# Kernel optimization log

Hardware: AMD Instinct MI355X
Metric: run time of the kernel (lower is better)

The kernel has to match this reference:

```python
import jax, jax.numpy as jnp
import numpy as np

ANCHORS = np.array([[10,13],[16,30],[33,23],[30,61],[62,45],[59,119],[116,90],[156,198],[373,326]], np.float32)
ANCHOR_MASK = [[6, 7, 8], [3, 4, 5], [0, 1, 2]]
INPUT_SHAPE = np.array([416, 416], np.float32)  # (h, w)
NUM_CLASSES = 80
EPS = 1e-7


def _bce(pred, target):
    # clip_by_tensor + binary cross entropy, as in the torch module
    p = jnp.clip(pred, EPS, 1.0 - EPS)
    return -target * jnp.log(p) - (1.0 - target) * jnp.log(1.0 - p)


def _box_iou(b1, b2):
    # b1: (..., 1, 4), b2: (..., n, 4), center-format xywh (normalized)
    b1_xy, b1_wh = b1[..., :2], b1[..., 2:4]
    b2_xy, b2_wh = b2[..., :2], b2[..., 2:4]
    b1_min, b1_max = b1_xy - b1_wh / 2.0, b1_xy + b1_wh / 2.0
    b2_min, b2_max = b2_xy - b2_wh / 2.0, b2_xy + b2_wh / 2.0
    inter_wh = jnp.maximum(jnp.minimum(b1_max, b2_max) - jnp.maximum(b1_min, b2_min), 0.0)
    inter = inter_wh[..., 0] * inter_wh[..., 1]
    a1 = b1_wh[..., 0] * b1_wh[..., 1]
    a2 = b2_wh[..., 0] * b2_wh[..., 1]
    return inter / (a1 + a2 - inter)


def _decode(y_pred, anchors):
    # y_pred: (b, 3*(5+C), h, w) -> raw: (b, 3, h, w, 5+C)
    b, _, h, w = y_pred.shape
    raw = y_pred.reshape(b, 3, 5 + NUM_CLASSES, h, w).transpose(0, 1, 3, 4, 2)
    gy, gx = jnp.meshgrid(jnp.arange(h, dtype=y_pred.dtype), jnp.arange(w, dtype=y_pred.dtype), indexing='ij')
    grid_xy = jnp.stack([gx, gy], axis=-1)  # (h, w, 2)
    pred_xy = jax.nn.sigmoid(raw[..., 0:2])
    pred_wh = raw[..., 2:4]                 # raw tw, th (MSE'd against log target)
    pred_conf = jax.nn.sigmoid(raw[..., 4:5])
    pred_class = jax.nn.sigmoid(raw[..., 5:])
    # decoded, normalized boxes for IoU-based negative mining
    box_xy = (pred_xy + grid_xy) / jnp.array([w, h], y_pred.dtype)
    box_wh = jnp.exp(pred_wh) * anchors.reshape(3, 1, 1, 2) / jnp.asarray(INPUT_SHAPE[::-1].copy())
    pred_box = jnp.concatenate([box_xy, box_wh], axis=-1)  # (b,3,h,w,4)
    return grid_xy, pred_box, pred_xy, pred_wh, pred_conf, pred_class


def _layer_loss(y_pred, y_true, target, anchors):
    b, _, h, w = y_pred.shape
    grid_xy, pred_box, pred_xy, pred_wh, pred_conf, pred_class = _decode(y_pred, anchors)
    object_mask = y_true[..., 4:5]
    true_xy = y_true[..., 0:2] * jnp.array([h, w], y_pred.dtype) - grid_xy
    true_wh = jnp.log(y_true[..., 2:4] * jnp.asarray(INPUT_SHAPE[::-1].copy()) / anchors.reshape(3, 1, 1, 2))
    true_wh = jnp.where(object_mask > 0, true_wh, jnp.zeros_like(true_wh))
    loss_scale = 2.0 - y_true[..., 2:3] * y_true[..., 3:4]
    # negative mask: every grid/anchor prediction vs all true boxes of its image (vectorized over batch)
    iou = _box_iou(pred_box[:, :, :, :, None, :], target[:, None, None, None, :, :4])  # (b,3,h,w,n)
    best_iou = jnp.max(iou, axis=-1)
    neg = (best_iou < 0.5).astype(y_pred.dtype)[..., None]
    neg_mask = (1.0 - object_mask) * neg
    loss_xy = jnp.sum(object_mask * loss_scale * _bce(pred_xy, true_xy))
    loss_wh = jnp.sum(object_mask * loss_scale * 0.5 * (pred_wh - true_wh) ** 2)
    conf_bce = _bce(pred_conf, object_mask)
    loss_conf = jnp.sum(object_mask * conf_bce) + jnp.sum(neg_mask * conf_bce)
    loss_cls = jnp.sum(object_mask * _bce(pred_class, y_true[..., 5:]))
    return loss_xy + loss_wh + loss_conf + loss_cls


def setup_inputs() -> dict:
    key = jax.random.key(0)
    ks = jax.random.split(key, 7)
    grids = [13, 26, 52]
    b, n = 32, 20
    inp = {}
    for i, g in enumerate(grids):
        inp[f'y_pred{i}'] = jax.random.normal(ks[i], (b, 3 * (5 + NUM_CLASSES), g, g), jnp.float32)
        # y_true values in (0.05, 0.95): keeps log(true_wh) and 1/y_true grads bounded
        inp[f'y_true{i}'] = 0.05 + 0.9 * jax.random.uniform(ks[3 + i], (b, 3, g, g, 5 + NUM_CLASSES), jnp.float32)
    inp['target'] = 0.05 + 0.9 * jax.random.uniform(ks[6], (b, n, 5), jnp.float32)
    return inp


def reference(y_pred0, y_pred1, y_pred2, y_true0, y_true1, y_true2, target):
    total = jnp.zeros((), jnp.float32)
    for yp, yt, mask in ((y_pred0, y_true0, ANCHOR_MASK[0]),
                         (y_pred1, y_true1, ANCHOR_MASK[1]),
                         (y_pred2, y_true2, ANCHOR_MASK[2])):
        total = total + _layer_loss(yp, yt, target, jnp.asarray(ANCHORS[mask]))
    return total
```

## Files before the change

### kernel.cpp

```cpp
#include <hip/hip_runtime.h>
#include <math.h>

#define BLOCK 256
#define NB0 64
#define NB1 254
#define NB2 1014
#define NBLOCKS (NB0 + NB1 + NB2)

typedef float f4a __attribute__((ext_vector_type(4), aligned(4)));

__constant__ float c_anch[9][2] = {
    {116.f, 90.f}, {156.f, 198.f}, {373.f, 326.f},
    { 30.f, 61.f}, { 62.f,  45.f}, { 59.f, 119.f},
    { 10.f, 13.f}, { 16.f,  30.f}, { 33.f,  23.f}
};

__device__ __forceinline__ float softplusf(float x) {
    float ax = fabsf(x);
    return fmaxf(x, 0.f) + __logf(1.f + __expf(-ax));
}

__device__ __forceinline__ float sigmoidf(float x) {
    return __fdividef(1.f, 1.f + __expf(-x));
}

__global__ __launch_bounds__(BLOCK, 8) void yolo_loss_main(
    const float* __restrict__ p0, const float* __restrict__ p1, const float* __restrict__ p2,
    const float* __restrict__ t0, const float* __restrict__ t1, const float* __restrict__ t2,
    const float* __restrict__ tgt, float* __restrict__ partials)
{
    __shared__ float sh[BLOCK][17];

    int blk = blockIdx.x;
    const float* pred;
    const float* tru;
    int layer, g, cells, bbase;
    if (blk < NB0)            { layer = 0; pred = p0; tru = t0; g = 13; cells = 16224;  bbase = 0; }
    else if (blk < NB0 + NB1) { layer = 1; pred = p1; tru = t1; g = 26; cells = 64896;  bbase = NB0; }
    else                      { layer = 2; pred = p2; tru = t2; g = 52; cells = 259584; bbase = NB0 + NB1; }

    int tid = threadIdx.x;
    int cell0 = (blk - bbase) * BLOCK;
    int idx = cell0 + tid;
    bool active = idx < cells;
    int nvalid = min(BLOCK, cells - cell0);
    const float* trow = tru + (size_t)cell0 * 85;

#pragma unroll
    for (int k = 0; k < 5; k++) {
        int f = k * BLOCK + tid;
        int cell = f / 5;
        int ch = f - cell * 5;
        int cc = min(cell, nvalid - 1);
        sh[cell][ch] = trow[(size_t)cc * 85 + ch];
    }
    __syncthreads();

    int cidx = active ? idx : (cells - 1);
    int hw = g * g;
    int ij = cidx % hw;
    int a  = (cidx / hw) % 3;
    int b  = cidx / (3 * hw);
    int i  = ij / g;
    int j  = ij - i * g;
    const float* pb = pred + (size_t)((b * 3 + a) * 85) * hw + ij;

    float acc = 0.f;
    float mask = 0.f;

    if (active) {
        float y0 = sh[tid][0], y1 = sh[tid][1], y2 = sh[tid][2], y3 = sh[tid][3];
        mask = sh[tid][4];

        float r0 = pb[0];
        float r1 = pb[hw];
        float r2 = pb[2 * hw];
        float r3 = pb[3 * hw];
        float r4 = pb[4 * hw];

        float gf = (float)g, gx = (float)j, gy = (float)i;
        float aw = c_anch[layer * 3 + a][0];
        float ah = c_anch[layer * 3 + a][1];

        float true_x = y0 * gf - gx;
        float true_y = y1 * gf - gy;
        float ls = 2.f - y2 * y3;
        float lxy = (softplusf(r0) - true_x * r0) + (softplusf(r1) - true_y * r1);
        acc += mask * ls * lxy;

        float tw = __logf(y2 * (416.f / aw));
        float th = __logf(y3 * (416.f / ah));
        float dw = r2 - tw, dh = r3 - th;
        acc += mask * ls * 0.5f * (dw * dw + dh * dh);

        float cbce = softplusf(r4) - mask * r4;

        float sx = sigmoidf(r0);
        float sy = sigmoidf(r1);
        float bx = __fdividef(sx + gx, gf);
        float by = __fdividef(sy + gy, gf);
        float bw = __expf(r2) * aw * (1.f / 416.f);
        float bh = __expf(r3) * ah * (1.f / 416.f);
        float a1 = bw * bh;
        float b1minx = bx - 0.5f * bw, b1maxx = bx + 0.5f * bw;
        float b1miny = by - 0.5f * bh, b1maxy = by + 0.5f * bh;

        const float* tg = tgt + b * 20 * 5;
        float best = 0.f;
#pragma unroll 5
        for (int k = 0; k < 20; k++) {
            f4a t = *reinterpret_cast<const f4a*>(tg + k * 5);
            float hw2 = 0.5f * t.z, hh2 = 0.5f * t.w;
            float iw = fminf(b1maxx, t.x + hw2) - fmaxf(b1minx, t.x - hw2);
            float ih = fminf(b1maxy, t.y + hh2) - fmaxf(b1miny, t.y - hh2);
            iw = fmaxf(iw, 0.f);
            ih = fmaxf(ih, 0.f);
            float inter = iw * ih;
            float iou = __fdividef(inter, a1 + t.z * t.w - inter);
            best = fmaxf(best, iou);
        }
        float neg = (best < 0.5f) ? 1.f : 0.f;
        acc += mask * cbce + (1.f - mask) * neg * cbce;
    }

    float cls = 0.f;
    for (int q = 0; q < 5; q++) {
        __syncthreads();
#pragma unroll
        for (int k = 0; k < 16; k++) {
            int f = k * BLOCK + tid;
            int cell = f >> 4;
            int ch = f & 15;
            int cc = min(cell, nvalid - 1);
            sh[cell][ch] = trow[(size_t)cc * 85 + 5 + q * 16 + ch];
        }
        __syncthreads();
        if (active) {
#pragma unroll
            for (int c = 0; c < 16; c++) {
                float x = pb[(size_t)(5 + q * 16 + c) * hw];
                float t = sh[tid][c];
                cls += softplusf(x) - t * x;
            }
        }
    }
    if (active) acc += mask * cls;

    for (int off = 32; off > 0; off >>= 1)
        acc += __shfl_down(acc, off, 64);
    __shared__ float shr[BLOCK / 64];
    if ((threadIdx.x & 63) == 0)
        shr[threadIdx.x >> 6] = acc;
    __syncthreads();
    if (threadIdx.x == 0) {
        float s = 0.f;
        for (int wv = 0; wv < BLOCK / 64; wv++) s += shr[wv];
        partials[blockIdx.x] = s;
    }
}

__global__ __launch_bounds__(BLOCK) void yolo_loss_reduce(
    const float* __restrict__ partials, float* __restrict__ out)
{
    float s = 0.f;
    for (int i = threadIdx.x; i < NBLOCKS; i += BLOCK)
        s += partials[i];
    for (int off = 32; off > 0; off >>= 1)
        s += __shfl_down(s, off, 64);
    __shared__ float sh[BLOCK / 64];
    if ((threadIdx.x & 63) == 0)
        sh[threadIdx.x >> 6] = s;
    __syncthreads();
    if (threadIdx.x == 0) {
        float tot = 0.f;
        for (int wv = 0; wv < BLOCK / 64; wv++) tot += sh[wv];
        out[0] = tot;
    }
}

extern "C" void kernel_launch(void* const* d_in, const int* in_sizes, int n_in,
                              void* d_out, int out_size, void* d_ws, size_t ws_size,
                              hipStream_t stream) {
    const float* p0  = (const float*)d_in[0];
    const float* t0  = (const float*)d_in[1];
    const float* p1  = (const float*)d_in[2];
    const float* t1  = (const float*)d_in[3];
    const float* p2  = (const float*)d_in[4];
    const float* t2  = (const float*)d_in[5];
    const float* tgt = (const float*)d_in[6];
    float* partials  = (float*)d_ws;

    yolo_loss_main<<<NBLOCKS, BLOCK, 0, stream>>>(p0, p1, p2, t0, t1, t2, tgt, partials);
    yolo_loss_reduce<<<1, BLOCK, 0, stream>>>(partials, (float*)d_out);
}
```

Before: 288.1 us.

## Software-pipeline y_true staging with register prefetch and double-buffered LDS

Restructures the y_true loading into six 16-channel stages, issuing global loads for the next stage into registers while the current stage is consumed from a second shared-memory buffer. This hides global load latency behind the class-loss compute and cuts the number of barriers per stage. In exchange it uses more registers and twice the LDS, and the launch bound drops from 8 to 4 blocks per CU, which lowers occupancy.

```diff
diff --git a/kernel.cpp b/kernel.cpp
--- a/kernel.cpp
+++ b/kernel.cpp
@@ -24,12 +24,56 @@
     return __fdividef(1.f, 1.f + __expf(-x));
 }
 
-__global__ __launch_bounds__(BLOCK, 8) void yolo_loss_main(
+
+template<int Q>
+__device__ __forceinline__ void stage_issue(const float* __restrict__ trow,
+                                            int tid, int nvalid, float* reg) {
+    constexpr int nch = (Q == 5) ? 5 : 16;
+#pragma unroll
+    for (int k = 0; k < nch; k++) {
+        int f = k * BLOCK + tid;
+        int cell = (Q == 5) ? (f / 5) : (f >> 4);
+        int ch = f - cell * nch;
+        int cc = min(cell, nvalid - 1);
+        reg[k] = trow[(size_t)cc * 85 + Q * 16 + ch];
+    }
+}
+
+template<int Q>
+__device__ __forceinline__ void stage_write(float (&sh)[BLOCK][17], int tid,
+                                            const float* reg) {
+    constexpr int nch = (Q == 5) ? 5 : 16;
+#pragma unroll
+    for (int k = 0; k < nch; k++) {
+        int f = k * BLOCK + tid;
+        int cell = (Q == 5) ? (f / 5) : (f >> 4);
+        int ch = f - cell * nch;
+        sh[cell][ch] = reg[k];
+    }
+}
+
+template<int Q>
+__device__ __forceinline__ float consume_cls(const float (&sh)[BLOCK][17],
+                                             const float* __restrict__ pb,
+                                             int tid, int hw) {
+    constexpr int nch = (Q == 5) ? 5 : 16;
+    float cls = 0.f;
+#pragma unroll
+    for (int c = 0; c < nch; c++) {
+        float x = pb[(size_t)(Q * 16 + c) * hw];
+        float t = sh[tid][c];
+        cls += softplusf(x) - t * x;
+    }
+    return cls;
+}
+
+__global__ __launch_bounds__(BLOCK, 4) void yolo_loss_main(
     const float* __restrict__ p0, const float* __restrict__ p1, const float* __restrict__ p2,
     const float* __restrict__ t0, const float* __restrict__ t1, const float* __restrict__ t2,
     const float* __restrict__ tgt, float* __restrict__ partials)
 {
-    __shared__ float sh[BLOCK][17];
+    __shared__ float shA[BLOCK][17];
+    __shared__ float shB[BLOCK][17];
 
     int blk = blockIdx.x;
     const float* pred;
@@ -45,16 +89,6 @@
     bool active = idx < cells;
     int nvalid = min(BLOCK, cells - cell0);
     const float* trow = tru + (size_t)cell0 * 85;
-
-#pragma unroll
-    for (int k = 0; k < 5; k++) {
-        int f = k * BLOCK + tid;
-        int cell = f / 5;
-        int ch = f - cell * 5;
-        int cc = min(cell, nvalid - 1);
-        sh[cell][ch] = trow[(size_t)cc * 85 + ch];
-    }
-    __syncthreads();
 
     int cidx = active ? idx : (cells - 1);
     int hw = g * g;
@@ -65,12 +99,19 @@
     int j  = ij - i * g;
     const float* pb = pred + (size_t)((b * 3 + a) * 85) * hw + ij;
 
-    float acc = 0.f;
-    float mask = 0.f;
-
+    float rA[16], rB[16];
+
+    stage_issue<0>(trow, tid, nvalid, rA);
+    stage_issue<1>(trow, tid, nvalid, rB);
+    stage_write<0>(shA, tid, rA);
+    __syncthreads();
+
+    float acc = 0.f, cls = 0.f, mask = 0.f;
+
+    stage_issue<2>(trow, tid, nvalid, rA);
     if (active) {
-        float y0 = sh[tid][0], y1 = sh[tid][1], y2 = sh[tid][2], y3 = sh[tid][3];
-        mask = sh[tid][4];
+        float y0 = shA[tid][0], y1 = shA[tid][1], y2 = shA[tid][2], y3 = shA[tid][3];
+        mask = shA[tid][4];
 
         float r0 = pb[0];
         float r1 = pb[hw];
@@ -121,30 +162,40 @@
         }
         float neg = (best < 0.5f) ? 1.f : 0.f;
         acc += mask * cbce + (1.f - mask) * neg * cbce;
-    }
-
-    float cls = 0.f;
-    for (int q = 0; q < 5; q++) {
-        __syncthreads();
-#pragma unroll
-        for (int k = 0; k < 16; k++) {
-            int f = k * BLOCK + tid;
-            int cell = f >> 4;
-            int ch = f & 15;
-            int cc = min(cell, nvalid - 1);
-            sh[cell][ch] = trow[(size_t)cc * 85 + 5 + q * 16 + ch];
+
+#pragma unroll
+        for (int c = 5; c < 16; c++) {
+            float x = pb[(size_t)c * hw];
+            float t = shA[tid][c];
+            cls += softplusf(x) - t * x;
         }
-        __syncthreads();
-        if (active) {
-#pragma unroll
-            for (int c = 0; c < 16; c++) {
-                float x = pb[(size_t)(5 + q * 16 + c) * hw];
-                float t = sh[tid][c];
-                cls += softplusf(x) - t * x;
-            }
-        }
-    }
-    if (active) acc += mask * cls;
+    }
+    stage_write<1>(shB, tid, rB);
+    __syncthreads();
+
+    stage_issue<3>(trow, tid, nvalid, rB);
+    if (active) cls += consume_cls<1>(shB, pb, tid, hw);
+    stage_write<2>(shA, tid, rA);
+    __syncthreads();
+
+    stage_issue<4>(trow, tid, nvalid, rA);
+    if (active) cls += consume_cls<2>(shA, pb, tid, hw);
+    stage_write<3>(shB, tid, rB);
+    __syncthreads();
+
+    stage_issue<5>(trow, tid, nvalid, rB);
+    if (active) cls += consume_cls<3>(shB, pb, tid, hw);
+    stage_write<4>(shA, tid, rA);
+    __syncthreads();
+
+    if (active) cls += consume_cls<4>(shA, pb, tid, hw);
+    stage_write<5>(shB, tid, rB);
+    __syncthreads();
+
+    if (active) {
+        cls += consume_cls<5>(shB, pb, tid, hw);
+        acc += mask * cls;
+    }
 
     for (int off = 32; off > 0; off >>= 1)
         acc += __shfl_down(acc, off, 64);
```

After: 275.5 us. -4.4%, faster.

## Stage class targets per wavefront with register prefetch instead of block barriers

Applied to the files above, without the earlier changes.

Each 64-lane wavefront now stages its own slice of y_true in a private shared-memory tile, so the per-chunk block-wide __syncthreads are gone. The next 16-channel class chunk is loaded into registers while the current chunk is consumed, overlapping global loads with the softplus work. Full wavefronts get an unclamped fast path for the strided reads. The register prefetch raises register pressure, so the launch-bounds occupancy hint drops from 8 to 6 blocks, and correctness now depends on in-wavefront ordering of LDS accesses without explicit barriers.

```diff
diff --git a/kernel.cpp b/kernel.cpp
--- a/kernel.cpp
+++ b/kernel.cpp
@@ -24,12 +24,50 @@
     return __fdividef(1.f, 1.f + __expf(-x));
 }
 
-__global__ __launch_bounds__(BLOCK, 8) void yolo_loss_main(
+
+template<int Q>
+__device__ __forceinline__ void stage_cls(const float* __restrict__ tw, int lane,
+                                          int nvc, bool full, float* r) {
+    if (full) {
+        int lo = (lane >> 4) * 85 + (lane & 15);
+#pragma unroll
+        for (int k = 0; k < 16; k++)
+            r[k] = tw[lo + k * 340 + 5 + Q * 16];
+    } else {
+#pragma unroll
+        for (int k = 0; k < 16; k++) {
+            int cc = min(k * 4 + (lane >> 4), nvc - 1);
+            r[k] = tw[cc * 85 + (lane & 15) + 5 + Q * 16];
+        }
+    }
+}
+
+__device__ __forceinline__ void write_cls(float (*S)[17], int lane, const float* r) {
+#pragma unroll
+    for (int k = 0; k < 16; k++)
+        S[k * 4 + (lane >> 4)][lane & 15] = r[k];
+}
+
+template<int Q>
+__device__ __forceinline__ float consume_cls(const float (*S)[17],
+                                             const float* __restrict__ pb,
+                                             int lane, int hw) {
+    float cls = 0.f;
+#pragma unroll
+    for (int c = 0; c < 16; c++) {
+        float x = pb[(size_t)((5 + Q * 16 + c) * hw)];
+        float t = S[lane][c];
+        cls += softplusf(x) - t * x;
+    }
+    return cls;
+}
+
+__global__ __launch_bounds__(BLOCK, 6) void yolo_loss_main(
     const float* __restrict__ p0, const float* __restrict__ p1, const float* __restrict__ p2,
     const float* __restrict__ t0, const float* __restrict__ t1, const float* __restrict__ t2,
     const float* __restrict__ tgt, float* __restrict__ partials)
 {
-    __shared__ float sh[BLOCK][17];
+    __shared__ float sh[4][64][17];
 
     int blk = blockIdx.x;
     const float* pred;
@@ -40,111 +78,128 @@
     else                      { layer = 2; pred = p2; tru = t2; g = 52; cells = 259584; bbase = NB0 + NB1; }
 
     int tid = threadIdx.x;
-    int cell0 = (blk - bbase) * BLOCK;
-    int idx = cell0 + tid;
-    bool active = idx < cells;
-    int nvalid = min(BLOCK, cells - cell0);
-    const float* trow = tru + (size_t)cell0 * 85;
-
-#pragma unroll
-    for (int k = 0; k < 5; k++) {
-        int f = k * BLOCK + tid;
-        int cell = f / 5;
-        int ch = f - cell * 5;
-        int cc = min(cell, nvalid - 1);
-        sh[cell][ch] = trow[(size_t)cc * 85 + ch];
-    }
-    __syncthreads();
-
-    int cidx = active ? idx : (cells - 1);
-    int hw = g * g;
-    int ij = cidx % hw;
-    int a  = (cidx / hw) % 3;
-    int b  = cidx / (3 * hw);
-    int i  = ij / g;
-    int j  = ij - i * g;
-    const float* pb = pred + (size_t)((b * 3 + a) * 85) * hw + ij;
-
+    int lane = tid & 63;
+    int wv = tid >> 6;
+    int cell0 = (blk - bbase) * BLOCK + wv * 64;
+    int nv = cells - cell0;
     float acc = 0.f;
-    float mask = 0.f;
-
-    if (active) {
-        float y0 = sh[tid][0], y1 = sh[tid][1], y2 = sh[tid][2], y3 = sh[tid][3];
-        mask = sh[tid][4];
-
-        float r0 = pb[0];
-        float r1 = pb[hw];
-        float r2 = pb[2 * hw];
-        float r3 = pb[3 * hw];
-        float r4 = pb[4 * hw];
-
-        float gf = (float)g, gx = (float)j, gy = (float)i;
-        float aw = c_anch[layer * 3 + a][0];
-        float ah = c_anch[layer * 3 + a][1];
-
-        float true_x = y0 * gf - gx;
-        float true_y = y1 * gf - gy;
-        float ls = 2.f - y2 * y3;
-        float lxy = (softplusf(r0) - true_x * r0) + (softplusf(r1) - true_y * r1);
-        acc += mask * ls * lxy;
-
-        float tw = __logf(y2 * (416.f / aw));
-        float th = __logf(y3 * (416.f / ah));
-        float dw = r2 - tw, dh = r3 - th;
-        acc += mask * ls * 0.5f * (dw * dw + dh * dh);
-
-        float cbce = softplusf(r4) - mask * r4;
-
-        float sx = sigmoidf(r0);
-        float sy = sigmoidf(r1);
-        float bx = __fdividef(sx + gx, gf);
-        float by = __fdividef(sy + gy, gf);
-        float bw = __expf(r2) * aw * (1.f / 416.f);
-        float bh = __expf(r3) * ah * (1.f / 416.f);
-        float a1 = bw * bh;
-        float b1minx = bx - 0.5f * bw, b1maxx = bx + 0.5f * bw;
-        float b1miny = by - 0.5f * bh, b1maxy = by + 0.5f * bh;
-
-        const float* tg = tgt + b * 20 * 5;
-        float best = 0.f;
+
+    if (nv > 0) {
+        float (*S)[17] = sh[wv];
+        bool full = (nv >= 64);
+        int nvc = full ? 64 : nv;
+        bool active = lane < nv;
+        const float* tw = tru + (size_t)cell0 * 85;
+
+        int cidx = active ? (cell0 + lane) : (cells - 1);
+        int hw = g * g;
+        int ij = cidx % hw;
+        int a  = (cidx / hw) % 3;
+        int b  = cidx / (3 * hw);
+        int i  = ij / g;
+        int j  = ij - i * g;
+        const float* pb = pred + (size_t)((b * 3 + a) * 85) * hw + ij;
+
+        {
+            float hreg[5];
+#pragma unroll
+            for (int k = 0; k < 5; k++) {
+                int f = k * 64 + lane;
+                int cell = f / 5;
+                int ch = f - cell * 5;
+                int cc = full ? cell : min(cell, nvc - 1);
+                hreg[k] = tw[cc * 85 + ch];
+            }
+#pragma unroll
+            for (int k = 0; k < 5; k++) {
+                int f = k * 64 + lane;
+                int cell = f / 5;
+                int ch = f - cell * 5;
+                S[cell][ch] = hreg[k];
+            }
+        }
+
+        float creg[16];
+        stage_cls<0>(tw, lane, nvc, full, creg);
+
+        float cls = 0.f, mask = 0.f;
+        if (active) {
+            float y0 = S[lane][0], y1 = S[lane][1], y2 = S[lane][2], y3 = S[lane][3];
+            mask = S[lane][4];
+
+            float r0 = pb[0];
+            float r1 = pb[hw];
+            float r2 = pb[2 * hw];
+            float r3 = pb[3 * hw];
+            float r4 = pb[4 * hw];
+
+            float gf = (float)g, gx = (float)j, gy = (float)i;
+            float aw = c_anch[layer * 3 + a][0];
+            float ah = c_anch[layer * 3 + a][1];
+
+            float true_x = y0 * gf - gx;
+            float true_y = y1 * gf - gy;
+            float ls = 2.f - y2 * y3;
+            float lxy = (softplusf(r0) - true_x * r0) + (softplusf(r1) - true_y * r1);
+            acc += mask * ls * lxy;
+
+            float tw_ = __logf(y2 * (416.f / aw));
+            float th_ = __logf(y3 * (416.f / ah));
+            float dw = r2 - tw_, dh = r3 - th_;
+            acc += mask * ls * 0.5f * (dw * dw + dh * dh);
+
+            float cbce = softplusf(r4) - mask * r4;
+
+            float sx = sigmoidf(r0);
+            float sy = sigmoidf(r1);
+            float bx = __fdividef(sx + gx, gf);
+            float by = __fdividef(sy + gy, gf);
+            float bw = __expf(r2) * aw * (1.f / 416.f);
+            float bh = __expf(r3) * ah * (1.f / 416.f);
+            float a1 = bw * bh;
+            float b1minx = bx - 0.5f * bw, b1maxx = bx + 0.5f * bw;
+            float b1miny = by - 0.5f * bh, b1maxy = by + 0.5f * bh;
+
+            const float* tg = tgt + b * 20 * 5;
+            float best = 0.f;
 #pragma unroll 5
-        for (int k = 0; k < 20; k++) {
-            f4a t = *reinterpret_cast<const f4a*>(tg + k * 5);
-            float hw2 = 0.5f * t.z, hh2 = 0.5f * t.w;
-            float iw = fminf(b1maxx, t.x + hw2) - fmaxf(b1minx, t.x - hw2);
-            float ih = fminf(b1maxy, t.y + hh2) - fmaxf(b1miny, t.y - hh2);
-            iw = fmaxf(iw, 0.f);
-            ih = fmaxf(ih, 0.f);
-            float inter = iw * ih;
-            float iou = __fdividef(inter, a1 + t.z * t.w - inter);
-            best = fmaxf(best, iou);
-        }
-        float neg = (best < 0.5f) ? 1.f : 0.f;
-        acc += mask * cbce + (1.f - mask) * neg * cbce;
-    }
-
-    float cls = 0.f;
-    for (int q = 0; q < 5; q++) {
-        __syncthreads();
-#pragma unroll
-        for (int k = 0; k < 16; k++) {
-            int f = k * BLOCK + tid;
-            int cell = f >> 4;
-            int ch = f & 15;
-            int cc = min(cell, nvalid - 1);
-            sh[cell][ch] = trow[(size_t)cc * 85 + 5 + q * 16 + ch];
-        }
-        __syncthreads();
+            for (int k = 0; k < 20; k++) {
+                f4a t = *reinterpret_cast<const f4a*>(tg + k * 5);
+                float hw2 = 0.5f * t.z, hh2 = 0.5f * t.w;
+                float iw = fminf(b1maxx, t.x + hw2) - fmaxf(b1minx, t.x - hw2);
+                float ih = fminf(b1maxy, t.y + hh2) - fmaxf(b1miny, t.y - hh2);
+                iw = fmaxf(iw, 0.f);
+                ih = fmaxf(ih, 0.f);
+                float inter = iw * ih;
+                float iou = __fdividef(inter, a1 + t.z * t.w - inter);
+                best = fmaxf(best, iou);
+            }
+            float neg = (best < 0.5f) ? 1.f : 0.f;
+            acc += mask * cbce + (1.f - mask) * neg * cbce;
+        }
+
+        write_cls(S, lane, creg);
+        stage_cls<1>(tw, lane, nvc, full, creg);
+        if (active) cls += consume_cls<0>(S, pb, lane, hw);
+
+        write_cls(S, lane, creg);
+        stage_cls<2>(tw, lane, nvc, full, creg);
+        if (active) cls += consume_cls<1>(S, pb, lane, hw);
+
+        write_cls(S, lane, creg);
+        stage_cls<3>(tw, lane, nvc, full, creg);
+        if (active) cls += consume_cls<2>(S, pb, lane, hw);
+
+        write_cls(S, lane, creg);
+        stage_cls<4>(tw, lane, nvc, full, creg);
+        if (active) cls += consume_cls<3>(S, pb, lane, hw);
+
+        write_cls(S, lane, creg);
         if (active) {
-#pragma unroll
-            for (int c = 0; c < 16; c++) {
-                float x = pb[(size_t)(5 + q * 16 + c) * hw];
-                float t = sh[tid][c];
-                cls += softplusf(x) - t * x;
-            }
-        }
-    }
-    if (active) acc += mask * cls;
+            cls += consume_cls<4>(S, pb, lane, hw);
+            acc += mask * cls;
+        }
+    }
 
     for (int off = 32; off > 0; off >>= 1)
         acc += __shfl_down(acc, off, 64);
@@ -154,7 +209,7 @@
     __syncthreads();
     if (threadIdx.x == 0) {
         float s = 0.f;
-        for (int wv = 0; wv < BLOCK / 64; wv++) s += shr[wv];
+        for (int w = 0; w < BLOCK / 64; w++) s += shr[w];
         partials[blockIdx.x] = s;
     }
 }
```

Measured after the change: 253.1 us. 1.14x faster.
